# Kernel tuning notes

Hardware: AMD Instinct MI355X
Metric: run time of the kernel (lower is better)

## Reference

```python
import jax, jax.numpy as jnp
import numpy as np
from jax import lax

D = 1024      # embed_dim
L = 8         # num_blocks
H = 8         # num_heads
P = 4         # patch_size
IMG = 64
B = 64
N = (IMG // P) ** 2 + 1   # 257 tokens (cls + patches)
DF = 4 * D
EPS = 1e-6


def _ln(x, g, b):
    m = jnp.mean(x, axis=-1, keepdims=True)
    v = jnp.var(x, axis=-1, keepdims=True)
    return (x - m) * jax.lax.rsqrt(v + EPS) * g + b


def setup_inputs() -> dict:
    key = jax.random.key(0)
    ks = jax.random.split(key, 20)
    s = 0.02
    return {
        "x": jax.random.normal(ks[0], (B, IMG, IMG, 3), jnp.float32),
        "conv_w": jax.random.normal(ks[1], (P, P, 3, D), jnp.float32) * s,
        "conv_b": jnp.zeros((D,), jnp.float32),
        "cls_token": jax.random.normal(ks[2], (1, 1, D), jnp.float32) * s,
        "pos_emb": jax.random.normal(ks[3], (N, D), jnp.float32) * s,
        "ln1_g": jnp.ones((L, D), jnp.float32),
        "ln1_b": jnp.zeros((L, D), jnp.float32),
        "wq": jax.random.normal(ks[4], (L, D, D), jnp.float32) * s,
        "wk": jax.random.normal(ks[5], (L, D, D), jnp.float32) * s,
        "wv": jax.random.normal(ks[6], (L, D, D), jnp.float32) * s,
        "proj_w": jax.random.normal(ks[7], (L, D, D), jnp.float32) * s,
        "proj_b": jnp.zeros((L, D), jnp.float32),
        "ln2_g": jnp.ones((L, D), jnp.float32),
        "ln2_b": jnp.zeros((L, D), jnp.float32),
        "mlp1_w": jax.random.normal(ks[8], (L, D, DF), jnp.float32) * s,
        "mlp1_b": jnp.zeros((L, DF), jnp.float32),
        "mlp2_w": jax.random.normal(ks[9], (L, DF, D), jnp.float32) * s,
        "mlp2_b": jnp.zeros((L, D), jnp.float32),
    }


def _forward(x, conv_w, conv_b, cls_token, pos_emb, ln1_g, ln1_b, wq, wk, wv,
             proj_w, proj_b, ln2_g, ln2_b, mlp1_w, mlp1_b, mlp2_w, mlp2_b):
    bsz = x.shape[0]
    # patch embedding: strided conv, NHWC / HWIO
    r = lax.conv_general_dilated(x, conv_w, (P, P), 'VALID',
                                 dimension_numbers=('NHWC', 'HWIO', 'NHWC')) + conv_b
    tokens = r.reshape(bsz, -1, D)                         # [B, 256, D]
    cls = jnp.broadcast_to(cls_token, (bsz, 1, D))
    t = jnp.concatenate([cls, tokens], axis=1) + pos_emb[None]   # [B, N, D]

    hd = D // H
    scale = hd ** -0.5
    for i in range(L):
        xn = _ln(t, ln1_g[i], ln1_b[i])
        q = (xn @ wq[i] * scale).reshape(bsz, N, H, hd)
        k = (xn @ wk[i]).reshape(bsz, N, H, hd)
        v = (xn @ wv[i]).reshape(bsz, N, H, hd)
        attn = jax.nn.softmax(jnp.einsum('bqhd,bkhd->bhqk', q, k), axis=-1)
        y = jnp.einsum('bhqk,bkhd->bqhd', attn, v).reshape(bsz, N, D)
        t = t + y @ proj_w[i] + proj_b[i]
        xn2 = _ln(t, ln2_g[i], ln2_b[i])
        h = jax.nn.gelu(xn2 @ mlp1_w[i] + mlp1_b[i], approximate=False)
        t = t + h @ mlp2_w[i] + mlp2_b[i]
    return t[:, 0]   # gp='none' -> cls token


def reference(x, conv_w, conv_b, cls_token, pos_emb, ln1_g, ln1_b, wq, wk, wv,
              proj_w, proj_b, ln2_g, ln2_b, mlp1_w, mlp1_b, mlp2_w, mlp2_b):
    return _forward(x, conv_w, conv_b, cls_token, pos_emb, ln1_g, ln1_b, wq, wk, wv,
                    proj_w, proj_b, ln2_g, ln2_b, mlp1_w, mlp1_b, mlp2_w, mlp2_b)
```

## Files before the change

kernel.cpp:

```cpp
#include <hip/hip_runtime.h>
#include <math.h>

typedef __bf16 bf16;
typedef __bf16 bf16x8 __attribute__((ext_vector_type(8)));
typedef __bf16 bf16x2v __attribute__((ext_vector_type(2)));
typedef float f32x4 __attribute__((ext_vector_type(4)));

#define DD     1024
#define NL     8
#define NTOK   257
#define NB     64
#define DFF    4096
#define MM     (NB*NTOK)
#define NP     288
#define HD     128
#define CHUNK  128

__device__ __forceinline__ void gld16(const void* g, void* l) {
  __builtin_amdgcn_global_load_lds((__attribute__((address_space(1))) void*)g,
                                   (__attribute__((address_space(3))) void*)l,
                                   16, 0, 0);
}

template<int NT, int NR>
__device__ __forceinline__ void stage_sw(const bf16* __restrict__ p, int ld,
                                         int row0, int rmax, int k0,
                                         char* lds, int t) {
  int wb = (t >> 6) << 10;
  int cs = ((((t & 3) - (t >> 3)) & 3) << 3);
  #pragma unroll
  for (int i = 0; i < (NR*4)/NT; ++i) {
    int r = row0 + i*(NT/4) + (t >> 2);
    r = r < rmax ? r : rmax;
    gld16(p + (long)r*ld + k0 + cs, lds + i*(NT*16) + wb);
  }
}

template<int NT, int BN>
__device__ __forceinline__ void gemm_core(const bf16* __restrict__ A, int lda, int ar0, int armax,
                                          const bf16* __restrict__ Bt, int ldb, int br0, int brmax,
                                          int K, f32x4 acc[4][4], char* lds) {
  int t = threadIdx.x;
  int lane = t & 63, w = t >> 6;
  int wr = (NT == 256 ? (w >> 1) : (w >> 2)) << 6;
  int wc = (NT == 256 ? (w & 1)  : (w & 3))  << 6;
  int ro = lane & 15, q = lane >> 4;
  int soff = ((q + (ro >> 1)) & 3) << 4;
  char* lA = lds;
  char* lB = lds + 8192;
  for (int k0 = 0; k0 < K; k0 += 32) {
    stage_sw<NT,128>(A,  lda, ar0, armax, k0, lA, t);
    stage_sw<NT,BN> (Bt, ldb, br0, brmax, k0, lB, t);
    __syncthreads();
    bf16x8 af[4], bfr[4];
    #pragma unroll
    for (int i = 0; i < 4; ++i)
      af[i]  = *(const bf16x8*)(lA + (wr + i*16 + ro)*64 + soff);
    #pragma unroll
    for (int j = 0; j < 4; ++j)
      bfr[j] = *(const bf16x8*)(lB + (wc + j*16 + ro)*64 + soff);
    #pragma unroll
    for (int i = 0; i < 4; ++i)
      #pragma unroll
      for (int j = 0; j < 4; ++j)
        acc[i][j] = __builtin_amdgcn_mfma_f32_16x16x32_bf16(af[i], bfr[j], acc[i][j], 0, 0, 0);
    __syncthreads();
  }
}

#define ACC_INIT f32x4 acc[4][4]; { f32x4 z = {0.f,0.f,0.f,0.f}; \
  for (int i=0;i<4;i++) for (int j=0;j<4;j++) acc[i][j]=z; }

#define EPILOG_IDX(NT) int te = threadIdx.x; int lane_ = te & 63; int w_ = te >> 6; \
  int r0 = ((NT==256 ? (w_>>1) : (w_>>2)) << 6) + ((lane_ >> 4) << 2); \
  int c0 = ((NT==256 ? (w_&1)  : (w_&3))  << 6) + (lane_ & 15);

__global__ void __launch_bounds__(512) k_gemm_qkv(const bf16* __restrict__ A,
    const bf16* __restrict__ Bt, bf16* __restrict__ qb, bf16* __restrict__ kb,
    bf16* __restrict__ vT) {
  __shared__ char lds[8192 + 256*64];
  ACC_INIT;
  gemm_core<512,256>(A, DD, blockIdx.x*128, MM-1, Bt, DD, blockIdx.y*256, 3071, DD, acc, lds);
  EPILOG_IDX(512);
  int mb = blockIdx.x*128, nb = blockIdx.y*256;
  #pragma unroll
  for (int i=0;i<4;i++)
    #pragma unroll
    for (int r=0;r<4;r++) {
      int m = mb + r0 + i*16 + r;
      if (m < MM) {
        unsigned bb = (unsigned)m / NTOK;
        int tok = m - (int)bb*NTOK;
        #pragma unroll
        for (int j=0;j<4;j++) {
          int n = nb + c0 + j*16;
          bf16 val = (bf16)acc[i][j][r];
          if (n < 2048) {
            (n < 1024 ? qb : kb)[(long)m*DD + (n & 1023)] = val;
          } else {
            int nv = n - 2048, h = nv >> 7, d = nv & 127;
            vT[(((long)(bb*8+h))*HD + d)*NP + tok] = val;
          }
        }
      }
    }
}

__global__ void __launch_bounds__(512) k_gemm_resid(const bf16* __restrict__ A,
    const bf16* __restrict__ Bt, const float* __restrict__ bias,
    float* __restrict__ T, int K) {
  __shared__ char lds[8192 + 256*64];
  ACC_INIT;
  gemm_core<512,256>(A, K, blockIdx.x*128, MM-1, Bt, K, blockIdx.y*256, 1023, K, acc, lds);
  EPILOG_IDX(512);
  int mb = blockIdx.x*128, nb = blockIdx.y*256;
  #pragma unroll
  for (int i=0;i<4;i++)
    #pragma unroll
    for (int r=0;r<4;r++) {
      int m = mb + r0 + i*16 + r;
      if (m < MM) {
        #pragma unroll
        for (int j=0;j<4;j++) {
          int n = nb + c0 + j*16;
          long idx = (long)m*DD + n;
          T[idx] = T[idx] + acc[i][j][r] + bias[n];
        }
      }
    }
}

__global__ void __launch_bounds__(512) k_gemm_gelu(const bf16* __restrict__ A,
    const bf16* __restrict__ Bt, const float* __restrict__ bias,
    bf16* __restrict__ Hb) {
  __shared__ char lds[8192 + 256*64];
  ACC_INIT;
  gemm_core<512,256>(A, DD, blockIdx.x*128, MM-1, Bt, DD, blockIdx.y*256, 4095, DD, acc, lds);
  EPILOG_IDX(512);
  int mb = blockIdx.x*128, nb = blockIdx.y*256;
  #pragma unroll
  for (int i=0;i<4;i++)
    #pragma unroll
    for (int r=0;r<4;r++) {
      int m = mb + r0 + i*16 + r;
      if (m < MM) {
        #pragma unroll
        for (int j=0;j<4;j++) {
          int n = nb + c0 + j*16;
          float vv = acc[i][j][r] + bias[n];
          float ge = 0.5f*vv*(1.f + erff(vv*0.70710678118654752f));
          Hb[(long)m*DFF + n] = (bf16)ge;
        }
      }
    }
}

__global__ void __launch_bounds__(256) k_attn_s(const bf16* __restrict__ q,
    const bf16* __restrict__ kk, bf16* __restrict__ P, int bh0) {
  __shared__ char lds[16384];
  int l = blockIdx.z; int bh = bh0 + l; int b = bh >> 3; int h = bh & 7;
  const bf16* Ab = q  + (long)b*NTOK*DD + h*HD;
  const bf16* Bb = kk + (long)b*NTOK*DD + h*HD;
  ACC_INIT;
  gemm_core<256,128>(Ab, DD, blockIdx.x*128, NTOK-1, Bb, DD, blockIdx.y*128, NTOK-1, HD, acc, lds);
  EPILOG_IDX(256);
  bf16* Pp = P + (long)l*NP*NP;
  int mb = blockIdx.x*128, nb = blockIdx.y*128;
  #pragma unroll
  for (int i=0;i<4;i++)
    #pragma unroll
    for (int r=0;r<4;r++) {
      int m = mb + r0 + i*16 + r;
      if (m < NTOK) {
        #pragma unroll
        for (int j=0;j<4;j++) {
          int n = nb + c0 + j*16;
          if (n < NTOK) Pp[(long)m*NP + n] = (bf16)acc[i][j][r];
        }
      }
    }
}

__global__ void __launch_bounds__(256) k_attn_pv(const bf16* __restrict__ P,
    const bf16* __restrict__ vT, bf16* __restrict__ y, int bh0) {
  __shared__ char lds[16384];
  int l = blockIdx.z; int bh = bh0 + l; int b = bh >> 3; int h = bh & 7;
  const bf16* Ab = P  + (long)l*NP*NP;
  const bf16* Bb = vT + (long)bh*HD*NP;
  ACC_INIT;
  gemm_core<256,128>(Ab, NP, blockIdx.x*128, NP-1, Bb, NP, 0, HD-1, NP, acc, lds);
  EPILOG_IDX(256);
  int mb = blockIdx.x*128;
  #pragma unroll
  for (int i=0;i<4;i++)
    #pragma unroll
    for (int r=0;r<4;r++) {
      int m = mb + r0 + i*16 + r;
      if (m < NTOK) {
        #pragma unroll
        for (int j=0;j<4;j++) {
          int n = c0 + j*16;
          y[((long)b*NTOK + m)*DD + h*HD + n] = (bf16)acc[i][j][r];
        }
      }
    }
}

__global__ void __launch_bounds__(256) k_ln(const float* __restrict__ T,
    const float* __restrict__ g, const float* __restrict__ be,
    bf16* __restrict__ out) {
  int row = blockIdx.x;
  const float4* x4 = (const float4*)(T + (long)row*DD);
  int t = threadIdx.x;
  float4 v = x4[t];
  float s  = v.x+v.y+v.z+v.w;
  float ss = v.x*v.x+v.y*v.y+v.z*v.z+v.w*v.w;
  #pragma unroll
  for (int o=32;o;o>>=1){ s += __shfl_down(s,o); ss += __shfl_down(ss,o); }
  __shared__ float rsum[4], rsq[4];
  int lane = t&63, w = t>>6;
  if (lane==0){ rsum[w]=s; rsq[w]=ss; }
  __syncthreads();
  float S  = rsum[0]+rsum[1]+rsum[2]+rsum[3];
  float SS = rsq[0]+rsq[1]+rsq[2]+rsq[3];
  float mean = S*(1.f/DD);
  float var  = SS*(1.f/DD) - mean*mean;
  float rs = rsqrtf(var + 1e-6f);
  float4 gg = ((const float4*)g)[t];
  float4 bb = ((const float4*)be)[t];
  bf16* o = out + (long)row*DD + t*4;
  o[0]=(bf16)((v.x-mean)*rs*gg.x+bb.x);
  o[1]=(bf16)((v.y-mean)*rs*gg.y+bb.y);
  o[2]=(bf16)((v.z-mean)*rs*gg.z+bb.z);
  o[3]=(bf16)((v.w-mean)*rs*gg.w+bb.w);
}

__global__ void __launch_bounds__(256) k_softmax(bf16* __restrict__ P) {
  int t = threadIdx.x, lane = t & 63, w = t >> 6;
  int row = blockIdx.x*4 + w;
  int l = row / NTOK, qq = row - l*NTOK;
  bf16* p = P + (long)l*NP*NP + (long)qq*NP;
  float v[5]; float mx = -1e30f;
  #pragma unroll
  for (int i=0;i<5;i++){
    int c = lane + i*64;
    v[i] = (c < NTOK) ? (float)p[c] : -1e30f;
    mx = fmaxf(mx, v[i]);
  }
  #pragma unroll
  for (int o=32;o;o>>=1) mx = fmaxf(mx, __shfl_xor(mx, o));
  float s = 0.f;
  #pragma unroll
  for (int i=0;i<5;i++){ v[i] = __expf(v[i]-mx); s += v[i]; }
  #pragma unroll
  for (int o=32;o;o>>=1) s += __shfl_xor(s, o);
  float inv = 1.f / s;
  #pragma unroll
  for (int i=0;i<5;i++){ int c = lane + i*64; if (c < NTOK) p[c] = (bf16)(v[i]*inv); }
  if (lane < NP-NTOK) p[NTOK+lane] = (bf16)0.f;
}

__global__ void __launch_bounds__(256) k_transpose64(const float* __restrict__ in,
    bf16* __restrict__ out, int R, int C, float scale) {
  __shared__ float tile[64][65];
  int c0 = blockIdx.x*64, r0 = blockIdx.y*64;
  int t = threadIdx.x;
  int tr = t >> 5, tc = (t & 31) * 2;
  #pragma unroll
  for (int i = 0; i < 8; ++i) {
    int r = r0 + tr + i*8;
    float2 v = *(const float2*)&in[(long)r*C + c0 + tc];
    tile[tr + i*8][tc] = v.x; tile[tr + i*8][tc+1] = v.y;
  }
  __syncthreads();
  #pragma unroll
  for (int i = 0; i < 8; ++i) {
    int c = c0 + tr + i*8;
    bf16x2v o;
    o.x = (bf16)(tile[tc  ][tr + i*8] * scale);
    o.y = (bf16)(tile[tc+1][tr + i*8] * scale);
    *(bf16x2v*)&out[(long)c*R + r0 + tc] = o;
  }
}

__global__ void __launch_bounds__(256) k_embed(const float* __restrict__ x,
    const float* __restrict__ cw, const float* __restrict__ cb,
    const float* __restrict__ cls, const float* __restrict__ pos,
    float* __restrict__ T) {
  int blk = blockIdx.x; int b = blk / NTOK, tok = blk - b*NTOK;
  long orow = (long)(b*NTOK + tok)*DD;
  int t = threadIdx.x;
  if (tok == 0) {
    #pragma unroll
    for (int i=0;i<4;i++){ int d=t+i*256; T[orow+d] = cls[d] + pos[d]; }
    return;
  }
  __shared__ float patch[48];
  int pi = tok-1, py = pi>>4, px = pi&15;
  if (t < 48) {
    int i = t/12, j = (t/3)&3, c = t%3;
    patch[t] = x[(((long)(b*64 + py*4 + i))*64 + px*4 + j)*3 + c];
  }
  __syncthreads();
  float a[4];
  #pragma unroll
  for (int i=0;i<4;i++) a[i] = cb[t+i*256];
  for (int p=0;p<48;p++){
    float pv = patch[p];
    const float* wrow = cw + p*DD;
    #pragma unroll
    for (int i=0;i<4;i++) a[i] += pv * wrow[t+i*256];
  }
  #pragma unroll
  for (int i=0;i<4;i++){ int d=t+i*256; T[orow+d] = a[i] + pos[(long)tok*DD+d]; }
}

__global__ void __launch_bounds__(256) k_out(const float* __restrict__ T,
                                             float* __restrict__ out) {
  int b = blockIdx.x, t = threadIdx.x;
  #pragma unroll
  for (int i=0;i<4;i++){
    int d = t + i*256;
    out[(long)b*DD + d] = T[(long)b*NTOK*DD + d];
  }
}

extern "C" void kernel_launch(void* const* d_in, const int* in_sizes, int n_in,
                              void* d_out, int out_size, void* d_ws, size_t ws_size,
                              hipStream_t stream) {
  const float* x      = (const float*)d_in[0];
  const float* conv_w = (const float*)d_in[1];
  const float* conv_b = (const float*)d_in[2];
  const float* cls    = (const float*)d_in[3];
  const float* pos    = (const float*)d_in[4];
  const float* ln1_g  = (const float*)d_in[5];
  const float* ln1_b  = (const float*)d_in[6];
  const float* wq     = (const float*)d_in[7];
  const float* wk     = (const float*)d_in[8];
  const float* wv     = (const float*)d_in[9];
  const float* proj_w = (const float*)d_in[10];
  const float* proj_b = (const float*)d_in[11];
  const float* ln2_g  = (const float*)d_in[12];
  const float* ln2_b  = (const float*)d_in[13];
  const float* mlp1_w = (const float*)d_in[14];
  const float* mlp1_b = (const float*)d_in[15];
  const float* mlp2_w = (const float*)d_in[16];
  const float* mlp2_b = (const float*)d_in[17];

  const size_t TBUF_OFF = 0;
  const size_t XN_OFF   = 67371008;
  const size_t C_OFF    = XN_OFF + 33685504;
  const size_t NEED     = C_OFF + 151519232;
  if (ws_size < NEED) return;

  char* base = (char*)d_ws;
  float* tbuf  = (float*)(base + TBUF_OFF);
  bf16*  xn    = (bf16*)(base + XN_OFF);
  char*  C     = base + C_OFF;
  bf16* wqkvT  = (bf16*)(C + 0);
  bf16* projT  = wqkvT;
  bf16* qb     = (bf16*)(C + 6291456);
  bf16* kb     = (bf16*)(C + 39976960);
  bf16* vT     = (bf16*)(C + 73662464);
  bf16* Pc     = (bf16*)(C + 111411200);
  bf16* m1T    = (bf16*)(C + 0);
  bf16* m2T    = (bf16*)(C + 8388608);
  bf16* hb     = (bf16*)(C + 16777216);

  const float qscale = 0.08838834764831845f;

  k_embed<<<MM, 256, 0, stream>>>(x, conv_w, conv_b, cls, pos, tbuf);

  for (int i = 0; i < NL; ++i) {
    const long wo = (long)i*DD*DD;
    k_transpose64<<<dim3(16,16), 256, 0, stream>>>(wq + wo, wqkvT,             DD, DD, qscale);
    k_transpose64<<<dim3(16,16), 256, 0, stream>>>(wk + wo, wqkvT + 1024*1024, DD, DD, 1.f);
    k_transpose64<<<dim3(16,16), 256, 0, stream>>>(wv + wo, wqkvT + 2*1024*1024, DD, DD, 1.f);
    k_ln<<<MM, 256, 0, stream>>>(tbuf, ln1_g + i*DD, ln1_b + i*DD, xn);
    k_gemm_qkv<<<dim3(129,12), 512, 0, stream>>>(xn, wqkvT, qb, kb, vT);
    k_transpose64<<<dim3(16,16), 256, 0, stream>>>(proj_w + wo, projT, DD, DD, 1.f);
    for (int c = 0; c < 512/CHUNK; ++c) {
      k_attn_s <<<dim3(3,3,CHUNK), 256, 0, stream>>>(qb, kb, Pc, c*CHUNK);
      k_softmax<<<(CHUNK*NTOK)/4, 256, 0, stream>>>(Pc);
      k_attn_pv<<<dim3(3,1,CHUNK), 256, 0, stream>>>(Pc, vT, xn, c*CHUNK);
    }
    k_gemm_resid<<<dim3(129,4), 512, 0, stream>>>(xn, projT, proj_b + i*DD, tbuf, DD);
    k_ln<<<MM, 256, 0, stream>>>(tbuf, ln2_g + i*DD, ln2_b + i*DD, xn);
    k_transpose64<<<dim3(64,16), 256, 0, stream>>>(mlp1_w + (long)i*DD*DFF, m1T, DD, DFF, 1.f);
    k_transpose64<<<dim3(16,64), 256, 0, stream>>>(mlp2_w + (long)i*DFF*DD, m2T, DFF, DD, 1.f);
    k_gemm_gelu <<<dim3(129,16), 512, 0, stream>>>(xn, m1T, mlp1_b + i*DFF, hb);
    k_gemm_resid<<<dim3(129,4),  512, 0, stream>>>(hb, m2T, mlp2_b + i*DD, tbuf, DFF);
  }

  k_out<<<NB, 256, 0, stream>>>(tbuf, (float*)d_out);
}
```

Measured before the change: 8.074 ms.

## Double-buffer LDS staging in GEMM core and swizzle block order across XCDs

The GEMM main loop now uses two LDS buffers, so the global-to-LDS loads for the next K-slice are issued while MFMAs run on the current slice, and one barrier per iteration is removed. The large GEMM kernels also remap block indices so consecutive tiles land on the same XCD, which should improve L2 reuse of shared A/B tiles. The cost is doubled LDS per block, which may lower occupancy.

Result: faster. 7.272 ms (-9.9%).

```diff
diff --git a/kernel.cpp b/kernel.cpp
--- a/kernel.cpp
+++ b/kernel.cpp
@@ -34,6 +34,33 @@
     r = r < rmax ? r : rmax;
     gld16(p + (long)r*ld + k0 + cs, lds + i*(NT*16) + wb);
   }
+}
+
+__device__ __forceinline__ void swz_xy(int& X, int& Y) {
+  int gx = gridDim.x, gy = gridDim.y;
+  int G = gx * gy;
+  int orig = blockIdx.y * gx + blockIdx.x;
+  int q = G >> 3, r = G & 7;
+  int xcd = orig & 7, j = orig >> 3;
+  int wg = (xcd < r ? xcd*(q+1) : r*(q+1) + (xcd-r)*q) + j;
+  X = wg / gy; Y = wg - (wg / gy) * gy;
+}
+
+__device__ __forceinline__ void frag_mfma(const char* cA, const char* cB,
+                                          int wr, int wc, int ro, int soff,
+                                          f32x4 acc[4][4]) {
+  bf16x8 af[4], bfr[4];
+  #pragma unroll
+  for (int i = 0; i < 4; ++i)
+    af[i]  = *(const bf16x8*)(cA + (wr + i*16 + ro)*64 + soff);
+  #pragma unroll
+  for (int j = 0; j < 4; ++j)
+    bfr[j] = *(const bf16x8*)(cB + (wc + j*16 + ro)*64 + soff);
+  #pragma unroll
+  for (int i = 0; i < 4; ++i)
+    #pragma unroll
+    for (int j = 0; j < 4; ++j)
+      acc[i][j] = __builtin_amdgcn_mfma_f32_16x16x32_bf16(af[i], bfr[j], acc[i][j], 0, 0, 0);
 }
 
 template<int NT, int BN>
@@ -46,26 +73,22 @@
   int wc = (NT == 256 ? (w & 1)  : (w & 3))  << 6;
   int ro = lane & 15, q = lane >> 4;
   int soff = ((q + (ro >> 1)) & 3) << 4;
-  char* lA = lds;
-  char* lB = lds + 8192;
-  for (int k0 = 0; k0 < K; k0 += 32) {
-    stage_sw<NT,128>(A,  lda, ar0, armax, k0, lA, t);
-    stage_sw<NT,BN> (Bt, ldb, br0, brmax, k0, lB, t);
+  constexpr int AB = 128*64;
+  constexpr int BB = BN*64;
+  char* lB = lds + 2*AB;
+
+  stage_sw<NT,128>(A,  lda, ar0, armax, 0, lds, t);
+  stage_sw<NT,BN> (Bt, ldb, br0, brmax, 0, lB,  t);
+  __syncthreads();
+  int cur = 0;
+  for (int k0 = 32; k0 < K; k0 += 32) {
+    stage_sw<NT,128>(A,  lda, ar0, armax, k0, lds + (cur^1)*AB, t);
+    stage_sw<NT,BN> (Bt, ldb, br0, brmax, k0, lB  + (cur^1)*BB, t);
+    frag_mfma(lds + cur*AB, lB + cur*BB, wr, wc, ro, soff, acc);
     __syncthreads();
-    bf16x8 af[4], bfr[4];
-    #pragma unroll
-    for (int i = 0; i < 4; ++i)
-      af[i]  = *(const bf16x8*)(lA + (wr + i*16 + ro)*64 + soff);
-    #pragma unroll
-    for (int j = 0; j < 4; ++j)
-      bfr[j] = *(const bf16x8*)(lB + (wc + j*16 + ro)*64 + soff);
-    #pragma unroll
-    for (int i = 0; i < 4; ++i)
-      #pragma unroll
-      for (int j = 0; j < 4; ++j)
-        acc[i][j] = __builtin_amdgcn_mfma_f32_16x16x32_bf16(af[i], bfr[j], acc[i][j], 0, 0, 0);
-    __syncthreads();
-  }
+    cur ^= 1;
+  }
+  frag_mfma(lds + cur*AB, lB + cur*BB, wr, wc, ro, soff, acc);
 }
 
 #define ACC_INIT f32x4 acc[4][4]; { f32x4 z = {0.f,0.f,0.f,0.f}; \
@@ -78,11 +101,12 @@
 __global__ void __launch_bounds__(512) k_gemm_qkv(const bf16* __restrict__ A,
     const bf16* __restrict__ Bt, bf16* __restrict__ qb, bf16* __restrict__ kb,
     bf16* __restrict__ vT) {
-  __shared__ char lds[8192 + 256*64];
+  __shared__ char lds[2*8192 + 2*16384];
+  int X, Y; swz_xy(X, Y);
   ACC_INIT;
-  gemm_core<512,256>(A, DD, blockIdx.x*128, MM-1, Bt, DD, blockIdx.y*256, 3071, DD, acc, lds);
+  gemm_core<512,256>(A, DD, X*128, MM-1, Bt, DD, Y*256, 3071, DD, acc, lds);
   EPILOG_IDX(512);
-  int mb = blockIdx.x*128, nb = blockIdx.y*256;
+  int mb = X*128, nb = Y*256;
   #pragma unroll
   for (int i=0;i<4;i++)
     #pragma unroll
@@ -109,11 +133,12 @@
 __global__ void __launch_bounds__(512) k_gemm_resid(const bf16* __restrict__ A,
     const bf16* __restrict__ Bt, const float* __restrict__ bias,
     float* __restrict__ T, int K) {
-  __shared__ char lds[8192 + 256*64];
+  __shared__ char lds[2*8192 + 2*16384];
+  int X, Y; swz_xy(X, Y);
   ACC_INIT;
-  gemm_core<512,256>(A, K, blockIdx.x*128, MM-1, Bt, K, blockIdx.y*256, 1023, K, acc, lds);
+  gemm_core<512,256>(A, K, X*128, MM-1, Bt, K, Y*256, 1023, K, acc, lds);
   EPILOG_IDX(512);
-  int mb = blockIdx.x*128, nb = blockIdx.y*256;
+  int mb = X*128, nb = Y*256;
   #pragma unroll
   for (int i=0;i<4;i++)
     #pragma unroll
@@ -133,11 +158,12 @@
 __global__ void __launch_bounds__(512) k_gemm_gelu(const bf16* __restrict__ A,
     const bf16* __restrict__ Bt, const float* __restrict__ bias,
     bf16* __restrict__ Hb) {
-  __shared__ char lds[8192 + 256*64];
+  __shared__ char lds[2*8192 + 2*16384];
+  int X, Y; swz_xy(X, Y);
   ACC_INIT;
-  gemm_core<512,256>(A, DD, blockIdx.x*128, MM-1, Bt, DD, blockIdx.y*256, 4095, DD, acc, lds);
+  gemm_core<512,256>(A, DD, X*128, MM-1, Bt, DD, Y*256, 4095, DD, acc, lds);
   EPILOG_IDX(512);
-  int mb = blockIdx.x*128, nb = blockIdx.y*256;
+  int mb = X*128, nb = Y*256;
   #pragma unroll
   for (int i=0;i<4;i++)
     #pragma unroll
@@ -157,7 +183,7 @@
 
 __global__ void __launch_bounds__(256) k_attn_s(const bf16* __restrict__ q,
     const bf16* __restrict__ kk, bf16* __restrict__ P, int bh0) {
-  __shared__ char lds[16384];
+  __shared__ char lds[2*8192 + 2*8192];
   int l = blockIdx.z; int bh = bh0 + l; int b = bh >> 3; int h = bh & 7;
   const bf16* Ab = q  + (long)b*NTOK*DD + h*HD;
   const bf16* Bb = kk + (long)b*NTOK*DD + h*HD;
@@ -183,7 +209,7 @@
 
 __global__ void __launch_bounds__(256) k_attn_pv(const bf16* __restrict__ P,
     const bf16* __restrict__ vT, bf16* __restrict__ y, int bh0) {
-  __shared__ char lds[16384];
+  __shared__ char lds[2*8192 + 2*8192];
   int l = blockIdx.z; int bh = bh0 + l; int b = bh >> 3; int h = bh & 7;
   const bf16* Ab = P  + (long)l*NP*NP;
   const bf16* Bb = vT + (long)bh*HD*NP;
```
